# Kernel tuning notes

Hardware: AMD Instinct MI355X
Metric: run time of the kernel (lower is better)

Reference implementation:

```python
import jax, jax.numpy as jnp
import numpy as np

N_NODES = 50000
E_EDGES = 800000
NODE_DIM = 64
HID = 128


def _leaky(x):
    return jnp.where(x > 0, x, 0.2 * x)


def _gat_conv(x, W, a_src, a_dst, b, src, dst, heads, out_ch, concat):
    # x: [N, in]; W: [in, heads*out]; a_src/a_dst: [heads, out]
    N = x.shape[0]
    h = (x @ W).reshape(N, heads, out_ch)            # [N, H, C]
    s = (h * a_src[None]).sum(-1)                    # [N, H]
    d = (h * a_dst[None]).sum(-1)                    # [N, H]
    e = _leaky(s[src] + d[dst])                      # [E, H]
    m = jax.ops.segment_max(e, dst, num_segments=N)  # segment softmax (stable)
    ex = jnp.exp(e - m[dst])
    denom = jax.ops.segment_sum(ex, dst, num_segments=N)
    alpha = ex / denom[dst]                          # [E, H] (self-loops -> denom>0)
    out = jax.ops.segment_sum(h[src] * alpha[..., None], dst, num_segments=N)
    out = out.reshape(N, heads * out_ch) if concat else out.mean(axis=1)
    return out + b


def setup_inputs() -> dict:
    key = jax.random.key(0)
    ks = jax.random.split(key, 16)
    sc = 0.1
    inp = {
        "x": jax.random.normal(ks[0], (N_NODES, NODE_DIM), jnp.float32),
        "edge_index": jax.random.randint(ks[1], (2, E_EDGES), 0, N_NODES, jnp.int64),
        "fc_w": jax.random.normal(ks[2], (NODE_DIM, HID), jnp.float32) * sc,
        "fc_b": jnp.zeros((HID,), jnp.float32),
        "W1": jax.random.normal(ks[3], (HID, 2 * HID), jnp.float32) * sc,
        "asrc1": jax.random.normal(ks[4], (2, HID), jnp.float32) * sc,
        "adst1": jax.random.normal(ks[5], (2, HID), jnp.float32) * sc,
        "b1": jnp.zeros((2 * HID,), jnp.float32),
        "Wm": jax.random.normal(ks[6], (4, 2 * HID, 2 * HID), jnp.float32) * sc,
        "asrcm": jax.random.normal(ks[7], (4, 2, HID), jnp.float32) * sc,
        "adstm": jax.random.normal(ks[8], (4, 2, HID), jnp.float32) * sc,
        "bm": jnp.zeros((4, 2 * HID), jnp.float32),
        "W6": jax.random.normal(ks[9], (2 * HID, HID), jnp.float32) * sc,
        "asrc6": jax.random.normal(ks[10], (1, HID), jnp.float32) * sc,
        "adst6": jax.random.normal(ks[11], (1, HID), jnp.float32) * sc,
        "b6": jnp.zeros((HID,), jnp.float32),
    }
    return inp


def reference(x, edge_index, fc_w, fc_b, W1, asrc1, adst1, b1,
              Wm, asrcm, adstm, bm, W6, asrc6, adst6, b6):
    N = x.shape[0]
    loops = jnp.arange(N, dtype=edge_index.dtype)
    src = jnp.concatenate([edge_index[0], loops])  # add_self_loops=True (PyG default)
    dst = jnp.concatenate([edge_index[1], loops])

    out = jax.nn.relu(x @ fc_w + fc_b)
    out = _gat_conv(out, W1, asrc1, adst1, b1, src, dst, 2, HID, True)
    for i in range(4):
        out = _gat_conv(out, Wm[i], asrcm[i], adstm[i], bm[i], src, dst, 2, HID, True)
    out = _gat_conv(out, W6, asrc6, adst6, b6, src, dst, 1, HID, True)
    return out
```

## Files before the change

kernel.cpp:

```cpp
#include <hip/hip_runtime.h>
#include <cstdint>
#include <cstddef>

#define NN 50000
#define EE 800000
#define ET 850000

typedef unsigned short ushort_t;
typedef unsigned int uint_t;
using frag_ab = __attribute__((ext_vector_type(8))) short;
using f32x4   = __attribute__((ext_vector_type(4))) float;

__device__ inline ushort_t f2b(float x) {
  union { float f; unsigned int u; } c; c.f = x;
  unsigned int u = c.u;
  u += 0x7fffu + ((u >> 16) & 1u);
  return (ushort_t)(u >> 16);
}
__device__ inline float b2f(uint_t u) {
  union { unsigned int u; float f; } c; c.u = u << 16;
  return c.f;
}

__global__ __launch_bounds__(256) void k_count(const int* __restrict__ edge,
                                               int* __restrict__ counts) {
  int e = blockIdx.x * 256 + threadIdx.x;
  if (e >= ET) return;
  int dd = (e < EE) ? edge[EE + e] : (e - EE);
  atomicAdd(&counts[dd], 1);
}

__global__ __launch_bounds__(1024) void k_scan1(const int* __restrict__ counts,
                                                int* __restrict__ scn,
                                                int* __restrict__ bsum) {
  __shared__ int tmp[1024];
  int tid = threadIdx.x;
  int idx = blockIdx.x * 1024 + tid;
  int v = (idx < NN) ? counts[idx] : 0;
  tmp[tid] = v;
  __syncthreads();
  for (int o = 1; o < 1024; o <<= 1) {
    int u = (tid >= o) ? tmp[tid - o] : 0;
    __syncthreads();
    tmp[tid] += u;
    __syncthreads();
  }
  if (idx < NN) scn[idx] = tmp[tid] - v;
  if (tid == 1023) bsum[blockIdx.x] = tmp[1023];
}

__global__ __launch_bounds__(64) void k_scan2(const int* __restrict__ bsum,
                                              int* __restrict__ boff) {
  int l = threadIdx.x;
  const int NB = (NN + 1023) / 1024;
  int v = (l < NB) ? bsum[l] : 0;
  int own = v;
  for (int o = 1; o < 64; o <<= 1) {
    int u = __shfl_up(v, o);
    if (l >= o) v += u;
  }
  if (l < NB) boff[l] = v - own;
}

__global__ __launch_bounds__(1024) void k_scan3(const int* __restrict__ scn,
                                                const int* __restrict__ boff,
                                                int* __restrict__ row_ptr,
                                                int* __restrict__ cursor) {
  int idx = blockIdx.x * 1024 + threadIdx.x;
  if (idx < NN) {
    int v = scn[idx] + boff[blockIdx.x];
    row_ptr[idx] = v;
    cursor[idx] = v;
  }
  if (idx == 0) row_ptr[NN] = ET;
}

__global__ __launch_bounds__(256) void k_fill(const int* __restrict__ edge,
                                              int* __restrict__ cursor,
                                              int* __restrict__ col_src) {
  int e = blockIdx.x * 256 + threadIdx.x;
  if (e >= ET) return;
  int ss, dd;
  if (e < EE) { ss = edge[e]; dd = edge[EE + e]; }
  else        { ss = dd = e - EE; }
  int pos = atomicAdd(&cursor[dd], 1);
  col_src[pos] = ss;
}

__global__ __launch_bounds__(256) void k_prep_w(const float* __restrict__ fc_w,
                                                const float* __restrict__ W1,
                                                const float* __restrict__ Wm,
                                                const float* __restrict__ W6,
                                                ushort_t* __restrict__ fcWt,
                                                ushort_t* __restrict__ W1t,
                                                ushort_t* __restrict__ Wmt,
                                                ushort_t* __restrict__ W6t) {
  int i = blockIdx.x * 256 + threadIdx.x;
  if (i < 128 * 64) { int n = i >> 6, k = i & 63; fcWt[i] = f2b(fc_w[k * 128 + n]); return; }
  i -= 128 * 64;
  if (i < 256 * 128) { int n = i >> 7, k = i & 127; W1t[i] = f2b(W1[k * 256 + n]); return; }
  i -= 256 * 128;
  if (i < 4 * 256 * 256) {
    int l = i >> 16, r2 = i & 65535, n = r2 >> 8, k = r2 & 255;
    Wmt[i] = f2b(Wm[(size_t)l * 65536 + k * 256 + n]); return;
  }
  i -= 4 * 256 * 256;
  if (i < 128 * 256) { int n = i >> 8, k = i & 255; W6t[i] = f2b(W6[k * 128 + n]); return; }
}

template<int ABF16, int RELU, int SD>
__global__ __launch_bounds__(256) void k_mfma_gemm(const void* __restrict__ A,
                                                   const ushort_t* __restrict__ Bt,
                                                   ushort_t* __restrict__ C,
                                                   int M, int K, int Nc,
                                                   const float* __restrict__ bias,
                                                   const float* __restrict__ a_src,
                                                   const float* __restrict__ a_dst,
                                                   float* __restrict__ sbuf,
                                                   float* __restrict__ dbuf,
                                                   int H) {
  __shared__ ushort_t As[128 * 40];
  __shared__ ushort_t Bs[128 * 40];
  __shared__ float sdred[128][2][2];
  int row0 = blockIdx.x * 128;
  int col0 = blockIdx.y * 128;
  int t = threadIdx.x;
  int lane = t & 63, w = t >> 6;
  int wr = w >> 1, wc = w & 1;
  int r = lane & 15, kg = lane >> 4;

  f32x4 acc[4][4];
#pragma unroll
  for (int m = 0; m < 4; ++m)
#pragma unroll
    for (int n = 0; n < 4; ++n) acc[m][n] = (f32x4){0.f, 0.f, 0.f, 0.f};

  for (int k0 = 0; k0 < K; k0 += 32) {
    __syncthreads();
    if (ABF16) {
#pragma unroll
      for (int rep = 0; rep < 2; ++rep) {
        int c = t + rep * 256;
        int row = c >> 2, kc = c & 3;
        int grow = row0 + row;
        if (grow < M) {
          uint4 v = *(const uint4*)&((const ushort_t*)A)[(size_t)grow * K + k0 + kc * 8];
          *(uint4*)&As[row * 40 + kc * 8] = v;
        }
      }
    } else {
#pragma unroll
      for (int rep = 0; rep < 4; ++rep) {
        int c = t + rep * 256;
        int row = c >> 3, kc = c & 7;
        int grow = row0 + row;
        if (grow < M) {
          float4 v = *(const float4*)&((const float*)A)[(size_t)grow * K + k0 + kc * 4];
          ushort4 u;
          u.x = f2b(v.x); u.y = f2b(v.y); u.z = f2b(v.z); u.w = f2b(v.w);
          *(ushort4*)&As[row * 40 + kc * 4] = u;
        }
      }
    }
#pragma unroll
    for (int rep = 0; rep < 2; ++rep) {
      int c = t + rep * 256;
      int row = c >> 2, kc = c & 3;
      uint4 v = *(const uint4*)&Bt[(size_t)(col0 + row) * K + k0 + kc * 8];
      *(uint4*)&Bs[row * 40 + kc * 8] = v;
    }
    __syncthreads();

    frag_ab a[4], b[4];
#pragma unroll
    for (int m = 0; m < 4; ++m)
      a[m] = *(const frag_ab*)&As[(wr * 64 + m * 16 + r) * 40 + kg * 8];
#pragma unroll
    for (int n = 0; n < 4; ++n)
      b[n] = *(const frag_ab*)&Bs[(wc * 64 + n * 16 + r) * 40 + kg * 8];
#pragma unroll
    for (int m = 0; m < 4; ++m)
#pragma unroll
      for (int n = 0; n < 4; ++n)
        acc[m][n] = __builtin_amdgcn_mfma_f32_16x16x32_bf16(a[m], b[n], acc[m][n], 0, 0, 0);
  }

  int head = blockIdx.y;
  float as_[4], ad_[4];
  if (SD) {
#pragma unroll
    for (int n = 0; n < 4; ++n) {
      int cloc = wc * 64 + n * 16 + r;
      as_[n] = a_src[head * 128 + cloc];
      ad_[n] = a_dst[head * 128 + cloc];
    }
  }

#pragma unroll
  for (int m = 0; m < 4; ++m) {
    int gr0 = row0 + wr * 64 + m * 16 + kg * 4;
#pragma unroll
    for (int q = 0; q < 4; ++q) {
      int grow = gr0 + q;
      float ps = 0.f, pd = 0.f;
      if (grow < M) {
#pragma unroll
        for (int n = 0; n < 4; ++n) {
          int gcol = col0 + wc * 64 + n * 16 + r;
          float val = acc[m][n][q];
          if (SD) { ps += val * as_[n]; pd += val * ad_[n]; }
          if (bias) val += bias[gcol];
          if (RELU) val = fmaxf(val, 0.f);
          C[(size_t)grow * Nc + gcol] = f2b(val);
        }
      }
      if (SD) {
#pragma unroll
        for (int o = 1; o < 16; o <<= 1) {
          ps += __shfl_xor(ps, o);
          pd += __shfl_xor(pd, o);
        }
        int row_loc = wr * 64 + m * 16 + kg * 4 + q;
        if (r == 0) { sdred[row_loc][wc][0] = ps; sdred[row_loc][wc][1] = pd; }
      }
    }
  }
  if (SD) {
    __syncthreads();
    int row = t >> 1, which = t & 1;
    int grow = row0 + row;
    if (grow < M) {
      float v = sdred[row][0][which] + sdred[row][1][which];
      float* dst = which ? dbuf : sbuf;
      dst[(size_t)grow * H + head] = v;
    }
  }
}

template<int H, int OUTBF>
__global__ __launch_bounds__(256) void k_agg(const ushort_t* __restrict__ h2,
                                             const float* __restrict__ s,
                                             const float* __restrict__ dv,
                                             const int* __restrict__ row_ptr,
                                             const int* __restrict__ col_src,
                                             const float* __restrict__ bias,
                                             void* __restrict__ out) {
  int wid = threadIdx.x >> 6, l = threadIdx.x & 63;
  int n = blockIdx.x * 4 + wid;
  if (n >= NN) return;
  int beg = row_ptr[n], end = row_ptr[n + 1];
  float dn0, dn1 = 0.f;
  if (H == 2) { float2 tdn = ((const float2*)dv)[n]; dn0 = tdn.x; dn1 = tdn.y; }
  else dn0 = dv[n];

  float m0 = -1e30f, d0 = 0.f, m1 = -1e30f, d1 = 0.f;
  for (int e = beg + l; e < end; e += 64) {
    int src = col_src[e];
    if (H == 2) {
      float2 sv = ((const float2*)s)[src];
      float x0 = sv.x + dn0; x0 = x0 > 0.f ? x0 : 0.2f * x0;
      if (x0 > m0) { d0 = d0 * __expf(m0 - x0) + 1.f; m0 = x0; } else d0 += __expf(x0 - m0);
      float x1 = sv.y + dn1; x1 = x1 > 0.f ? x1 : 0.2f * x1;
      if (x1 > m1) { d1 = d1 * __expf(m1 - x1) + 1.f; m1 = x1; } else d1 += __expf(x1 - m1);
    } else {
      float x0 = s[src] + dn0; x0 = x0 > 0.f ? x0 : 0.2f * x0;
      if (x0 > m0) { d0 = d0 * __expf(m0 - x0) + 1.f; m0 = x0; } else d0 += __expf(x0 - m0);
    }
  }
#pragma unroll
  for (int o = 1; o < 64; o <<= 1) {
    float mo = __shfl_xor(m0, o), dno = __shfl_xor(d0, o);
    float M2 = fmaxf(m0, mo);
    d0 = d0 * __expf(m0 - M2) + dno * __expf(mo - M2);
    m0 = M2;
    if (H == 2) {
      mo = __shfl_xor(m1, o); dno = __shfl_xor(d1, o);
      M2 = fmaxf(m1, mo);
      d1 = d1 * __expf(m1 - M2) + dno * __expf(mo - M2);
      m1 = M2;
    }
  }

  if (H == 2) {
    const uint2* hrow = (const uint2*)h2;
    int hh = l >> 5;
    float a0 = 0.f, a1 = 0.f, a2 = 0.f, a3 = 0.f;
    for (int c = beg; c < end; c += 32) {
      int cnt = min(32, end - c);
      float alpv = 0.f; int srcv = 0;
      if (l < 2 * cnt) {
        int e = c + (l >> 1), hi = l & 1;
        srcv = col_src[e];
        float x = s[srcv * 2 + hi] + (hi ? dn1 : dn0);
        x = x > 0.f ? x : 0.2f * x;
        alpv = __expf(x - (hi ? m1 : m0));
      }
      int e = 0;
      for (; e + 4 <= cnt; e += 4) {
        float p0 = __shfl(alpv, 2 * e + hh);     int s0 = __shfl(srcv, 2 * e);
        float p1 = __shfl(alpv, 2 * e + 2 + hh); int s1 = __shfl(srcv, 2 * e + 2);
        float p2 = __shfl(alpv, 2 * e + 4 + hh); int s2 = __shfl(srcv, 2 * e + 4);
        float p3 = __shfl(alpv, 2 * e + 6 + hh); int s3 = __shfl(srcv, 2 * e + 6);
        uint2 v0 = hrow[(size_t)s0 * 64 + l];
        uint2 v1 = hrow[(size_t)s1 * 64 + l];
        uint2 v2 = hrow[(size_t)s2 * 64 + l];
        uint2 v3 = hrow[(size_t)s3 * 64 + l];
        a0 += p0 * b2f(v0.x & 0xffffu); a1 += p0 * b2f(v0.x >> 16);
        a2 += p0 * b2f(v0.y & 0xffffu); a3 += p0 * b2f(v0.y >> 16);
        a0 += p1 * b2f(v1.x & 0xffffu); a1 += p1 * b2f(v1.x >> 16);
        a2 += p1 * b2f(v1.y & 0xffffu); a3 += p1 * b2f(v1.y >> 16);
        a0 += p2 * b2f(v2.x & 0xffffu); a1 += p2 * b2f(v2.x >> 16);
        a2 += p2 * b2f(v2.y & 0xffffu); a3 += p2 * b2f(v2.y >> 16);
        a0 += p3 * b2f(v3.x & 0xffffu); a1 += p3 * b2f(v3.x >> 16);
        a2 += p3 * b2f(v3.y & 0xffffu); a3 += p3 * b2f(v3.y >> 16);
      }
      for (; e < cnt; ++e) {
        float p = __shfl(alpv, 2 * e + hh); int sc = __shfl(srcv, 2 * e);
        uint2 v = hrow[(size_t)sc * 64 + l];
        a0 += p * b2f(v.x & 0xffffu); a1 += p * b2f(v.x >> 16);
        a2 += p * b2f(v.y & 0xffffu); a3 += p * b2f(v.y >> 16);
      }
    }
    float dh = hh ? d1 : d0;
    float4 bb = ((const float4*)bias)[l];
    float o0 = a0 / dh + bb.x, o1 = a1 / dh + bb.y;
    float o2 = a2 / dh + bb.z, o3 = a3 / dh + bb.w;
    if (OUTBF) {
      uint2 ov;
      ov.x = (uint_t)f2b(o0) | ((uint_t)f2b(o1) << 16);
      ov.y = (uint_t)f2b(o2) | ((uint_t)f2b(o3) << 16);
      ((uint2*)out)[(size_t)n * 64 + l] = ov;
    } else {
      ((float4*)out)[(size_t)n * 64 + l] = make_float4(o0, o1, o2, o3);
    }
  } else {
    const uint_t* hrow = (const uint_t*)h2;
    float a0 = 0.f, a1 = 0.f;
    for (int c = beg; c < end; c += 64) {
      int cnt = min(64, end - c);
      float alpv = 0.f; int srcv = 0;
      if (l < cnt) {
        srcv = col_src[c + l];
        float x = s[srcv] + dn0;
        x = x > 0.f ? x : 0.2f * x;
        alpv = __expf(x - m0);
      }
      int e = 0;
      for (; e + 4 <= cnt; e += 4) {
        float p0 = __shfl(alpv, e);     int s0 = __shfl(srcv, e);
        float p1 = __shfl(alpv, e + 1); int s1 = __shfl(srcv, e + 1);
        float p2 = __shfl(alpv, e + 2); int s2 = __shfl(srcv, e + 2);
        float p3 = __shfl(alpv, e + 3); int s3 = __shfl(srcv, e + 3);
        uint_t v0 = hrow[(size_t)s0 * 64 + l];
        uint_t v1 = hrow[(size_t)s1 * 64 + l];
        uint_t v2 = hrow[(size_t)s2 * 64 + l];
        uint_t v3 = hrow[(size_t)s3 * 64 + l];
        a0 += p0 * b2f(v0 & 0xffffu); a1 += p0 * b2f(v0 >> 16);
        a0 += p1 * b2f(v1 & 0xffffu); a1 += p1 * b2f(v1 >> 16);
        a0 += p2 * b2f(v2 & 0xffffu); a1 += p2 * b2f(v2 >> 16);
        a0 += p3 * b2f(v3 & 0xffffu); a1 += p3 * b2f(v3 >> 16);
      }
      for (; e < cnt; ++e) {
        float p = __shfl(alpv, e); int sc = __shfl(srcv, e);
        uint_t v = hrow[(size_t)sc * 64 + l];
        a0 += p * b2f(v & 0xffffu); a1 += p * b2f(v >> 16);
      }
    }
    float2 bb = ((const float2*)bias)[l];
    float o0 = a0 / d0 + bb.x, o1 = a1 / d0 + bb.y;
    if (OUTBF) {
      ((uint_t*)out)[(size_t)n * 64 + l] = (uint_t)f2b(o0) | ((uint_t)f2b(o1) << 16);
    } else {
      ((float2*)out)[(size_t)n * 64 + l] = make_float2(o0, o1);
    }
  }
}

extern "C" void kernel_launch(void* const* d_in, const int* in_sizes, int n_in,
                              void* d_out, int out_size, void* d_ws, size_t ws_size,
                              hipStream_t stream) {
  const float* x     = (const float*)d_in[0];
  const int*   edge  = (const int*)d_in[1];
  const float* fc_w  = (const float*)d_in[2];
  const float* fc_b  = (const float*)d_in[3];
  const float* W1    = (const float*)d_in[4];
  const float* asrc1 = (const float*)d_in[5];
  const float* adst1 = (const float*)d_in[6];
  const float* b1    = (const float*)d_in[7];
  const float* Wm    = (const float*)d_in[8];
  const float* asrcm = (const float*)d_in[9];
  const float* adstm = (const float*)d_in[10];
  const float* bm    = (const float*)d_in[11];
  const float* W6    = (const float*)d_in[12];
  const float* asrc6 = (const float*)d_in[13];
  const float* adst6 = (const float*)d_in[14];
  const float* b6    = (const float*)d_in[15];

  char* w = (char*)d_ws;
  size_t off = 0;
  auto carve = [&](size_t bytes) -> char* {
    char* p = w + off;
    off = (off + bytes + 255) & ~(size_t)255;
    return p;
  };
  ushort_t* feat0 = (ushort_t*)carve((size_t)NN * 256 * 2);
  ushort_t* feat1 = (ushort_t*)carve((size_t)NN * 256 * 2);
  ushort_t* hbuf  = (ushort_t*)carve((size_t)NN * 256 * 2);
  float* sbuf   = (float*)carve((size_t)NN * 2 * 4);
  float* dbuf   = (float*)carve((size_t)NN * 2 * 4);
  ushort_t* fcWt = (ushort_t*)carve((size_t)128 * 64 * 2);
  ushort_t* W1t  = (ushort_t*)carve((size_t)256 * 128 * 2);
  ushort_t* Wmt  = (ushort_t*)carve((size_t)4 * 256 * 256 * 2);
  ushort_t* W6t  = (ushort_t*)carve((size_t)128 * 256 * 2);
  int* counts   = (int*)carve((size_t)NN * 4);
  int* row_ptr  = (int*)carve((size_t)(NN + 1) * 4);
  int* cursor   = (int*)carve((size_t)NN * 4);
  int* col_src  = (int*)carve((size_t)ET * 4);
  int* scn      = (int*)carve((size_t)NN * 4);
  int* bsum     = (int*)carve((size_t)64 * 4);
  int* boff     = (int*)carve((size_t)64 * 4);
  (void)ws_size;

  k_prep_w<<<(335872 + 255) / 256, 256, 0, stream>>>(fc_w, W1, Wm, W6, fcWt, W1t, Wmt, W6t);

  hipMemsetAsync(counts, 0, (size_t)NN * 4, stream);
  int eb = (ET + 255) / 256;
  const int NB = (NN + 1023) / 1024;
  k_count<<<eb, 256, 0, stream>>>(edge, counts);
  k_scan1<<<NB, 1024, 0, stream>>>(counts, scn, bsum);
  k_scan2<<<1, 64, 0, stream>>>(bsum, boff);
  k_scan3<<<NB, 1024, 0, stream>>>(scn, boff, row_ptr, cursor);
  k_fill<<<eb, 256, 0, stream>>>(edge, cursor, col_src);

  dim3 g1((NN + 127) / 128, 1), g2((NN + 127) / 128, 2);
  int ab = (NN + 3) / 4;

  auto gat = [&](const ushort_t* in, int K, const ushort_t* Wt, const float* a_s,
                 const float* a_d, const float* bias, void* outp, int H, int outbf) {
    k_mfma_gemm<1, 0, 1><<<(H == 2 ? g2 : g1), 256, 0, stream>>>(
        in, Wt, hbuf, NN, K, H * 128, nullptr, a_s, a_d, sbuf, dbuf, H);
    if (H == 2) {
      if (outbf)
        k_agg<2, 1><<<ab, 256, 0, stream>>>(hbuf, sbuf, dbuf, row_ptr, col_src, bias, outp);
      else
        k_agg<2, 0><<<ab, 256, 0, stream>>>(hbuf, sbuf, dbuf, row_ptr, col_src, bias, outp);
    } else {
      if (outbf)
        k_agg<1, 1><<<ab, 256, 0, stream>>>(hbuf, sbuf, dbuf, row_ptr, col_src, bias, outp);
      else
        k_agg<1, 0><<<ab, 256, 0, stream>>>(hbuf, sbuf, dbuf, row_ptr, col_src, bias, outp);
    }
  };

  k_mfma_gemm<0, 1, 0><<<g1, 256, 0, stream>>>(x, fcWt, feat0, NN, 64, 128, fc_b,
                                               nullptr, nullptr, nullptr, nullptr, 1);

  gat(feat0, 128, W1t, asrc1, adst1, b1, feat1, 2, 1);

  const ushort_t* cur = feat1;
  ushort_t* nxt = feat0;
  for (int i = 0; i < 4; ++i) {
    gat(cur, 256, Wmt + (size_t)i * 256 * 256, asrcm + (size_t)i * 2 * 128,
        adstm + (size_t)i * 2 * 128, bm + (size_t)i * 256, nxt, 2, 1);
    const ushort_t* tmp = cur;
    cur = nxt;
    nxt = (ushort_t*)tmp;
  }

  gat(cur, 256, W6t, asrc6, adst6, b6, d_out, 1, 0);
}
```

Baseline: 659.1 us.

## Use direct-to-LDS loads with swizzle in GEMM and 16-byte gathers in aggregation

The bf16 GEMM now uses K-tiles of 64 and loads A/B tiles straight into LDS with global_load_lds. Those tiles use an XOR-swizzled layout in place of padding, to cut register staging and LDS bank conflicts. The aggregation kernels now gather 16-byte rows per lane, with two or four edges processed in parallel across half- or quarter-wavefronts, then reduce across lanes with shuffles. This aims to lower the number of memory transactions in the edge gather, at the cost of an extra cross-lane reduction and idle lanes at the final store.

```diff
diff --git a/kernel.cpp b/kernel.cpp
--- a/kernel.cpp
+++ b/kernel.cpp
@@ -20,6 +20,12 @@
 __device__ inline float b2f(uint_t u) {
   union { unsigned int u; float f; } c; c.u = u << 16;
   return c.f;
+}
+
+__device__ inline void gload16(const ushort_t* g, ushort_t* l) {
+  __builtin_amdgcn_global_load_lds(
+      (const __attribute__((address_space(1))) unsigned int*)g,
+      (__attribute__((address_space(3))) unsigned int*)l, 16, 0, 0);
 }
 
 __global__ __launch_bounds__(256) void k_count(const int* __restrict__ edge,
@@ -108,19 +114,92 @@
   if (i < 128 * 256) { int n = i >> 8, k = i & 255; W6t[i] = f2b(W6[k * 128 + n]); return; }
 }
 
-template<int ABF16, int RELU, int SD>
-__global__ __launch_bounds__(256) void k_mfma_gemm(const void* __restrict__ A,
-                                                   const ushort_t* __restrict__ Bt,
-                                                   ushort_t* __restrict__ C,
-                                                   int M, int K, int Nc,
-                                                   const float* __restrict__ bias,
-                                                   const float* __restrict__ a_src,
-                                                   const float* __restrict__ a_dst,
-                                                   float* __restrict__ sbuf,
-                                                   float* __restrict__ dbuf,
-                                                   int H) {
+__global__ __launch_bounds__(256) void k_gemm_f32(const float* __restrict__ A,
+                                                  const ushort_t* __restrict__ Bt,
+                                                  ushort_t* __restrict__ C,
+                                                  int M, int K, int Nc,
+                                                  const float* __restrict__ bias) {
   __shared__ ushort_t As[128 * 40];
   __shared__ ushort_t Bs[128 * 40];
+  int row0 = blockIdx.x * 128;
+  int col0 = blockIdx.y * 128;
+  int t = threadIdx.x;
+  int lane = t & 63, w = t >> 6;
+  int wr = w >> 1, wc = w & 1;
+  int r = lane & 15, kg = lane >> 4;
+
+  f32x4 acc[4][4];
+#pragma unroll
+  for (int m = 0; m < 4; ++m)
+#pragma unroll
+    for (int n = 0; n < 4; ++n) acc[m][n] = (f32x4){0.f, 0.f, 0.f, 0.f};
+
+  for (int k0 = 0; k0 < K; k0 += 32) {
+    __syncthreads();
+#pragma unroll
+    for (int rep = 0; rep < 4; ++rep) {
+      int c = t + rep * 256;
+      int row = c >> 3, kc = c & 7;
+      int grow = row0 + row;
+      if (grow < M) {
+        float4 v = *(const float4*)&A[(size_t)grow * K + k0 + kc * 4];
+        ushort4 u;
+        u.x = f2b(v.x); u.y = f2b(v.y); u.z = f2b(v.z); u.w = f2b(v.w);
+        *(ushort4*)&As[row * 40 + kc * 4] = u;
+      }
+    }
+#pragma unroll
+    for (int rep = 0; rep < 2; ++rep) {
+      int c = t + rep * 256;
+      int row = c >> 2, kc = c & 3;
+      uint4 v = *(const uint4*)&Bt[(size_t)(col0 + row) * K + k0 + kc * 8];
+      *(uint4*)&Bs[row * 40 + kc * 8] = v;
+    }
+    __syncthreads();
+
+    frag_ab a[4], b[4];
+#pragma unroll
+    for (int m = 0; m < 4; ++m)
+      a[m] = *(const frag_ab*)&As[(wr * 64 + m * 16 + r) * 40 + kg * 8];
+#pragma unroll
+    for (int n = 0; n < 4; ++n)
+      b[n] = *(const frag_ab*)&Bs[(wc * 64 + n * 16 + r) * 40 + kg * 8];
+#pragma unroll
+    for (int m = 0; m < 4; ++m)
+#pragma unroll
+      for (int n = 0; n < 4; ++n)
+        acc[m][n] = __builtin_amdgcn_mfma_f32_16x16x32_bf16(a[m], b[n], acc[m][n], 0, 0, 0);
+  }
+
+#pragma unroll
+  for (int m = 0; m < 4; ++m) {
+    int gr0 = row0 + wr * 64 + m * 16 + kg * 4;
+#pragma unroll
+    for (int q = 0; q < 4; ++q) {
+      int grow = gr0 + q;
+      if (grow >= M) continue;
+#pragma unroll
+      for (int n = 0; n < 4; ++n) {
+        int gcol = col0 + wc * 64 + n * 16 + r;
+        float val = acc[m][n][q] + bias[gcol];
+        val = fmaxf(val, 0.f);
+        C[(size_t)grow * Nc + gcol] = f2b(val);
+      }
+    }
+  }
+}
+
+__global__ __launch_bounds__(256) void k_gemm64(const ushort_t* __restrict__ A,
+                                                const ushort_t* __restrict__ Bt,
+                                                ushort_t* __restrict__ C,
+                                                int M, int K, int Nc,
+                                                const float* __restrict__ a_src,
+                                                const float* __restrict__ a_dst,
+                                                float* __restrict__ sbuf,
+                                                float* __restrict__ dbuf,
+                                                int H) {
+  __shared__ ushort_t As[128 * 64];
+  __shared__ ushort_t Bs[128 * 64];
   __shared__ float sdred[128][2][2];
   int row0 = blockIdx.x * 128;
   int col0 = blockIdx.y * 128;
@@ -135,65 +214,51 @@
 #pragma unroll
     for (int n = 0; n < 4; ++n) acc[m][n] = (f32x4){0.f, 0.f, 0.f, 0.f};
 
-  for (int k0 = 0; k0 < K; k0 += 32) {
+  for (int k0 = 0; k0 < K; k0 += 64) {
     __syncthreads();
-    if (ABF16) {
-#pragma unroll
-      for (int rep = 0; rep < 2; ++rep) {
-        int c = t + rep * 256;
-        int row = c >> 2, kc = c & 3;
-        int grow = row0 + row;
-        if (grow < M) {
-          uint4 v = *(const uint4*)&((const ushort_t*)A)[(size_t)grow * K + k0 + kc * 8];
-          *(uint4*)&As[row * 40 + kc * 8] = v;
-        }
+#pragma unroll
+    for (int i = 0; i < 4; ++i) {
+      int c = w * 4 + i;
+      int b = c * 1024 + lane * 16;
+      int row = b >> 7;
+      int ks = ((b >> 4) & 7) ^ (row & 7);
+      const ushort_t* ga = A + (size_t)(row0 + row) * K + k0 + ks * 8;
+      if (row0 + row < M) gload16(ga, &As[c * 512]);
+      const ushort_t* gb = Bt + (size_t)(col0 + row) * K + k0 + ks * 8;
+      gload16(gb, &Bs[c * 512]);
+    }
+    __syncthreads();
+
+#pragma unroll
+    for (int kk = 0; kk < 2; ++kk) {
+      frag_ab af[4], bf[4];
+#pragma unroll
+      for (int m = 0; m < 4; ++m) {
+        int row = wr * 64 + m * 16 + r;
+        int byte = row * 128 + ((kk * 64 + kg * 16) ^ ((row & 7) << 4));
+        af[m] = *(const frag_ab*)((const char*)As + byte);
       }
-    } else {
-#pragma unroll
-      for (int rep = 0; rep < 4; ++rep) {
-        int c = t + rep * 256;
-        int row = c >> 3, kc = c & 7;
-        int grow = row0 + row;
-        if (grow < M) {
-          float4 v = *(const float4*)&((const float*)A)[(size_t)grow * K + k0 + kc * 4];
-          ushort4 u;
-          u.x = f2b(v.x); u.y = f2b(v.y); u.z = f2b(v.z); u.w = f2b(v.w);
-          *(ushort4*)&As[row * 40 + kc * 4] = u;
-        }
+#pragma unroll
+      for (int n = 0; n < 4; ++n) {
+        int row = wc * 64 + n * 16 + r;
+        int byte = row * 128 + ((kk * 64 + kg * 16) ^ ((row & 7) << 4));
+        bf[n] = *(const frag_ab*)((const char*)Bs + byte);
       }
-    }
-#pragma unroll
-    for (int rep = 0; rep < 2; ++rep) {
-      int c = t + rep * 256;
-      int row = c >> 2, kc = c & 3;
-      uint4 v = *(const uint4*)&Bt[(size_t)(col0 + row) * K + k0 + kc * 8];
-      *(uint4*)&Bs[row * 40 + kc * 8] = v;
-    }
-    __syncthreads();
-
-    frag_ab a[4], b[4];
-#pragma unroll
-    for (int m = 0; m < 4; ++m)
-      a[m] = *(const frag_ab*)&As[(wr * 64 + m * 16 + r) * 40 + kg * 8];
-#pragma unroll
-    for (int n = 0; n < 4; ++n)
-      b[n] = *(const frag_ab*)&Bs[(wc * 64 + n * 16 + r) * 40 + kg * 8];
-#pragma unroll
-    for (int m = 0; m < 4; ++m)
-#pragma unroll
-      for (int n = 0; n < 4; ++n)
-        acc[m][n] = __builtin_amdgcn_mfma_f32_16x16x32_bf16(a[m], b[n], acc[m][n], 0, 0, 0);
+#pragma unroll
+      for (int m = 0; m < 4; ++m)
+#pragma unroll
+        for (int n = 0; n < 4; ++n)
+          acc[m][n] = __builtin_amdgcn_mfma_f32_16x16x32_bf16(af[m], bf[n], acc[m][n], 0, 0, 0);
+    }
   }
 
   int head = blockIdx.y;
   float as_[4], ad_[4];
-  if (SD) {
-#pragma unroll
-    for (int n = 0; n < 4; ++n) {
-      int cloc = wc * 64 + n * 16 + r;
-      as_[n] = a_src[head * 128 + cloc];
-      ad_[n] = a_dst[head * 128 + cloc];
-    }
+#pragma unroll
+  for (int n = 0; n < 4; ++n) {
+    int cloc = wc * 64 + n * 16 + r;
+    as_[n] = a_src[head * 128 + cloc];
+    ad_[n] = a_dst[head * 128 + cloc];
   }
 
 #pragma unroll
@@ -208,64 +273,51 @@
         for (int n = 0; n < 4; ++n) {
           int gcol = col0 + wc * 64 + n * 16 + r;
           float val = acc[m][n][q];
-          if (SD) { ps += val * as_[n]; pd += val * ad_[n]; }
-          if (bias) val += bias[gcol];
-          if (RELU) val = fmaxf(val, 0.f);
+          ps += val * as_[n]; pd += val * ad_[n];
           C[(size_t)grow * Nc + gcol] = f2b(val);
         }
       }
-      if (SD) {
-#pragma unroll
-        for (int o = 1; o < 16; o <<= 1) {
-          ps += __shfl_xor(ps, o);
-          pd += __shfl_xor(pd, o);
-        }
-        int row_loc = wr * 64 + m * 16 + kg * 4 + q;
-        if (r == 0) { sdred[row_loc][wc][0] = ps; sdred[row_loc][wc][1] = pd; }
+#pragma unroll
+      for (int o = 1; o < 16; o <<= 1) {
+        ps += __shfl_xor(ps, o);
+        pd += __shfl_xor(pd, o);
       }
-    }
-  }
-  if (SD) {
-    __syncthreads();
-    int row = t >> 1, which = t & 1;
-    int grow = row0 + row;
-    if (grow < M) {
-      float v = sdred[row][0][which] + sdred[row][1][which];
-      float* dst = which ? dbuf : sbuf;
-      dst[(size_t)grow * H + head] = v;
-    }
-  }
-}
-
-template<int H, int OUTBF>
-__global__ __launch_bounds__(256) void k_agg(const ushort_t* __restrict__ h2,
-                                             const float* __restrict__ s,
-                                             const float* __restrict__ dv,
-                                             const int* __restrict__ row_ptr,
-                                             const int* __restrict__ col_src,
-                                             const float* __restrict__ bias,
-                                             void* __restrict__ out) {
+      int row_loc = wr * 64 + m * 16 + kg * 4 + q;
+      if (r == 0) { sdred[row_loc][wc][0] = ps; sdred[row_loc][wc][1] = pd; }
+    }
+  }
+  __syncthreads();
+  int row = t >> 1, which = t & 1;
+  int grow = row0 + row;
+  if (grow < M) {
+    float v = sdred[row][0][which] + sdred[row][1][which];
+    float* dst = which ? dbuf : sbuf;
+    dst[(size_t)grow * H + head] = v;
+  }
+}
+
+__global__ __launch_bounds__(256) void k_agg2(const ushort_t* __restrict__ h2,
+                                              const float* __restrict__ s,
+                                              const float* __restrict__ dv,
+                                              const int* __restrict__ row_ptr,
+                                              const int* __restrict__ col_src,
+                                              const float* __restrict__ bias,
+                                              uint4* __restrict__ out) {
   int wid = threadIdx.x >> 6, l = threadIdx.x & 63;
   int n = blockIdx.x * 4 + wid;
   if (n >= NN) return;
   int beg = row_ptr[n], end = row_ptr[n + 1];
-  float dn0, dn1 = 0.f;
-  if (H == 2) { float2 tdn = ((const float2*)dv)[n]; dn0 = tdn.x; dn1 = tdn.y; }
-  else dn0 = dv[n];
+  float2 tdn = ((const float2*)dv)[n];
+  float dn0 = tdn.x, dn1 = tdn.y;
 
   float m0 = -1e30f, d0 = 0.f, m1 = -1e30f, d1 = 0.f;
   for (int e = beg + l; e < end; e += 64) {
     int src = col_src[e];
-    if (H == 2) {
-      float2 sv = ((const float2*)s)[src];
-      float x0 = sv.x + dn0; x0 = x0 > 0.f ? x0 : 0.2f * x0;
-      if (x0 > m0) { d0 = d0 * __expf(m0 - x0) + 1.f; m0 = x0; } else d0 += __expf(x0 - m0);
-      float x1 = sv.y + dn1; x1 = x1 > 0.f ? x1 : 0.2f * x1;
-      if (x1 > m1) { d1 = d1 * __expf(m1 - x1) + 1.f; m1 = x1; } else d1 += __expf(x1 - m1);
-    } else {
-      float x0 = s[src] + dn0; x0 = x0 > 0.f ? x0 : 0.2f * x0;
-      if (x0 > m0) { d0 = d0 * __expf(m0 - x0) + 1.f; m0 = x0; } else d0 += __expf(x0 - m0);
-    }
+    float2 sv = ((const float2*)s)[src];
+    float x0 = sv.x + dn0; x0 = x0 > 0.f ? x0 : 0.2f * x0;
+    if (x0 > m0) { d0 = d0 * __expf(m0 - x0) + 1.f; m0 = x0; } else d0 += __expf(x0 - m0);
+    float x1 = sv.y + dn1; x1 = x1 > 0.f ? x1 : 0.2f * x1;
+    if (x1 > m1) { d1 = d1 * __expf(m1 - x1) + 1.f; m1 = x1; } else d1 += __expf(x1 - m1);
   }
 #pragma unroll
   for (int o = 1; o < 64; o <<= 1) {
@@ -273,106 +325,147 @@
     float M2 = fmaxf(m0, mo);
     d0 = d0 * __expf(m0 - M2) + dno * __expf(mo - M2);
     m0 = M2;
-    if (H == 2) {
-      mo = __shfl_xor(m1, o); dno = __shfl_xor(d1, o);
-      M2 = fmaxf(m1, mo);
-      d1 = d1 * __expf(m1 - M2) + dno * __expf(mo - M2);
-      m1 = M2;
-    }
-  }
-
-  if (H == 2) {
-    const uint2* hrow = (const uint2*)h2;
-    int hh = l >> 5;
-    float a0 = 0.f, a1 = 0.f, a2 = 0.f, a3 = 0.f;
-    for (int c = beg; c < end; c += 32) {
-      int cnt = min(32, end - c);
-      float alpv = 0.f; int srcv = 0;
-      if (l < 2 * cnt) {
-        int e = c + (l >> 1), hi = l & 1;
-        srcv = col_src[e];
-        float x = s[srcv * 2 + hi] + (hi ? dn1 : dn0);
-        x = x > 0.f ? x : 0.2f * x;
-        alpv = __expf(x - (hi ? m1 : m0));
-      }
-      int e = 0;
-      for (; e + 4 <= cnt; e += 4) {
-        float p0 = __shfl(alpv, 2 * e + hh);     int s0 = __shfl(srcv, 2 * e);
-        float p1 = __shfl(alpv, 2 * e + 2 + hh); int s1 = __shfl(srcv, 2 * e + 2);
-        float p2 = __shfl(alpv, 2 * e + 4 + hh); int s2 = __shfl(srcv, 2 * e + 4);
-        float p3 = __shfl(alpv, 2 * e + 6 + hh); int s3 = __shfl(srcv, 2 * e + 6);
-        uint2 v0 = hrow[(size_t)s0 * 64 + l];
-        uint2 v1 = hrow[(size_t)s1 * 64 + l];
-        uint2 v2 = hrow[(size_t)s2 * 64 + l];
-        uint2 v3 = hrow[(size_t)s3 * 64 + l];
-        a0 += p0 * b2f(v0.x & 0xffffu); a1 += p0 * b2f(v0.x >> 16);
-        a2 += p0 * b2f(v0.y & 0xffffu); a3 += p0 * b2f(v0.y >> 16);
-        a0 += p1 * b2f(v1.x & 0xffffu); a1 += p1 * b2f(v1.x >> 16);
-        a2 += p1 * b2f(v1.y & 0xffffu); a3 += p1 * b2f(v1.y >> 16);
-        a0 += p2 * b2f(v2.x & 0xffffu); a1 += p2 * b2f(v2.x >> 16);
-        a2 += p2 * b2f(v2.y & 0xffffu); a3 += p2 * b2f(v2.y >> 16);
-        a0 += p3 * b2f(v3.x & 0xffffu); a1 += p3 * b2f(v3.x >> 16);
-        a2 += p3 * b2f(v3.y & 0xffffu); a3 += p3 * b2f(v3.y >> 16);
-      }
-      for (; e < cnt; ++e) {
-        float p = __shfl(alpv, 2 * e + hh); int sc = __shfl(srcv, 2 * e);
-        uint2 v = hrow[(size_t)sc * 64 + l];
-        a0 += p * b2f(v.x & 0xffffu); a1 += p * b2f(v.x >> 16);
-        a2 += p * b2f(v.y & 0xffffu); a3 += p * b2f(v.y >> 16);
-      }
-    }
-    float dh = hh ? d1 : d0;
-    float4 bb = ((const float4*)bias)[l];
-    float o0 = a0 / dh + bb.x, o1 = a1 / dh + bb.y;
-    float o2 = a2 / dh + bb.z, o3 = a3 / dh + bb.w;
-    if (OUTBF) {
-      uint2 ov;
-      ov.x = (uint_t)f2b(o0) | ((uint_t)f2b(o1) << 16);
-      ov.y = (uint_t)f2b(o2) | ((uint_t)f2b(o3) << 16);
-      ((uint2*)out)[(size_t)n * 64 + l] = ov;
-    } else {
-      ((float4*)out)[(size_t)n * 64 + l] = make_float4(o0, o1, o2, o3);
-    }
-  } else {
-    const uint_t* hrow = (const uint_t*)h2;
-    float a0 = 0.f, a1 = 0.f;
-    for (int c = beg; c < end; c += 64) {
-      int cnt = min(64, end - c);
-      float alpv = 0.f; int srcv = 0;
-      if (l < cnt) {
-        srcv = col_src[c + l];
-        float x = s[srcv] + dn0;
-        x = x > 0.f ? x : 0.2f * x;
-        alpv = __expf(x - m0);
-      }
-      int e = 0;
-      for (; e + 4 <= cnt; e += 4) {
-        float p0 = __shfl(alpv, e);     int s0 = __shfl(srcv, e);
-        float p1 = __shfl(alpv, e + 1); int s1 = __shfl(srcv, e + 1);
-        float p2 = __shfl(alpv, e + 2); int s2 = __shfl(srcv, e + 2);
-        float p3 = __shfl(alpv, e + 3); int s3 = __shfl(srcv, e + 3);
-        uint_t v0 = hrow[(size_t)s0 * 64 + l];
-        uint_t v1 = hrow[(size_t)s1 * 64 + l];
-        uint_t v2 = hrow[(size_t)s2 * 64 + l];
-        uint_t v3 = hrow[(size_t)s3 * 64 + l];
-        a0 += p0 * b2f(v0 & 0xffffu); a1 += p0 * b2f(v0 >> 16);
-        a0 += p1 * b2f(v1 & 0xffffu); a1 += p1 * b2f(v1 >> 16);
-        a0 += p2 * b2f(v2 & 0xffffu); a1 += p2 * b2f(v2 >> 16);
-        a0 += p3 * b2f(v3 & 0xffffu); a1 += p3 * b2f(v3 >> 16);
-      }
-      for (; e < cnt; ++e) {
-        float p = __shfl(alpv, e); int sc = __shfl(srcv, e);
-        uint_t v = hrow[(size_t)sc * 64 + l];
-        a0 += p * b2f(v & 0xffffu); a1 += p * b2f(v >> 16);
-      }
-    }
-    float2 bb = ((const float2*)bias)[l];
-    float o0 = a0 / d0 + bb.x, o1 = a1 / d0 + bb.y;
-    if (OUTBF) {
-      ((uint_t*)out)[(size_t)n * 64 + l] = (uint_t)f2b(o0) | ((uint_t)f2b(o1) << 16);
-    } else {
-      ((float2*)out)[(size_t)n * 64 + l] = make_float2(o0, o1);
-    }
+    mo = __shfl_xor(m1, o); dno = __shfl_xor(d1, o);
+    M2 = fmaxf(m1, mo);
+    d1 = d1 * __expf(m1 - M2) + dno * __expf(mo - M2);
+    m1 = M2;
+  }
+
+  int hw = l >> 5, lh = l & 31;
+  int hd = lh >> 4;
+  const uint4* hrow = (const uint4*)h2;
+  float a0 = 0.f, a1 = 0.f, a2 = 0.f, a3 = 0.f;
+  float a4 = 0.f, a5 = 0.f, a6 = 0.f, a7 = 0.f;
+
+  for (int c = beg; c < end; c += 32) {
+    int cnt = min(32, end - c);
+    float alpv = 0.f; int srcv = 0;
+    if (l < 2 * cnt) {
+      int e = c + (l >> 1), hi = l & 1;
+      srcv = col_src[e];
+      float x = s[srcv * 2 + hi] + (hi ? dn1 : dn0);
+      x = x > 0.f ? x : 0.2f * x;
+      alpv = __expf(x - (hi ? m1 : m0));
+    }
+    int e = 0;
+    for (; e + 4 <= cnt + 1; e += 4) {
+      int ep0 = e + hw, ep1 = e + 2 + hw;
+      int s0 = __shfl(srcv, 2 * ep0);
+      int s1 = __shfl(srcv, 2 * ep1);
+      float p0 = __shfl(alpv, 2 * ep0 + hd);
+      float p1 = __shfl(alpv, 2 * ep1 + hd);
+      if (ep0 >= cnt) p0 = 0.f;
+      if (ep1 >= cnt) p1 = 0.f;
+      uint4 v0 = hrow[(size_t)s0 * 32 + lh];
+      uint4 v1 = hrow[(size_t)s1 * 32 + lh];
+      a0 = fmaf(p0, b2f(v0.x & 0xffffu), a0); a1 = fmaf(p0, b2f(v0.x >> 16), a1);
+      a2 = fmaf(p0, b2f(v0.y & 0xffffu), a2); a3 = fmaf(p0, b2f(v0.y >> 16), a3);
+      a4 = fmaf(p0, b2f(v0.z & 0xffffu), a4); a5 = fmaf(p0, b2f(v0.z >> 16), a5);
+      a6 = fmaf(p0, b2f(v0.w & 0xffffu), a6); a7 = fmaf(p0, b2f(v0.w >> 16), a7);
+      a0 = fmaf(p1, b2f(v1.x & 0xffffu), a0); a1 = fmaf(p1, b2f(v1.x >> 16), a1);
+      a2 = fmaf(p1, b2f(v1.y & 0xffffu), a2); a3 = fmaf(p1, b2f(v1.y >> 16), a3);
+      a4 = fmaf(p1, b2f(v1.z & 0xffffu), a4); a5 = fmaf(p1, b2f(v1.z >> 16), a5);
+      a6 = fmaf(p1, b2f(v1.w & 0xffffu), a6); a7 = fmaf(p1, b2f(v1.w >> 16), a7);
+    }
+    for (; e < cnt; e += 2) {
+      int ep = e + hw;
+      int s0 = __shfl(srcv, 2 * ep);
+      float p = __shfl(alpv, 2 * ep + hd);
+      if (ep >= cnt) p = 0.f;
+      uint4 v = hrow[(size_t)s0 * 32 + lh];
+      a0 = fmaf(p, b2f(v.x & 0xffffu), a0); a1 = fmaf(p, b2f(v.x >> 16), a1);
+      a2 = fmaf(p, b2f(v.y & 0xffffu), a2); a3 = fmaf(p, b2f(v.y >> 16), a3);
+      a4 = fmaf(p, b2f(v.z & 0xffffu), a4); a5 = fmaf(p, b2f(v.z >> 16), a5);
+      a6 = fmaf(p, b2f(v.w & 0xffffu), a6); a7 = fmaf(p, b2f(v.w >> 16), a7);
+    }
+  }
+  a0 += __shfl_xor(a0, 32); a1 += __shfl_xor(a1, 32);
+  a2 += __shfl_xor(a2, 32); a3 += __shfl_xor(a3, 32);
+  a4 += __shfl_xor(a4, 32); a5 += __shfl_xor(a5, 32);
+  a6 += __shfl_xor(a6, 32); a7 += __shfl_xor(a7, 32);
+
+  if (hw == 0) {
+    float dh = hd ? d1 : d0;
+    float inv = 1.f / dh;
+    float4 b0 = ((const float4*)bias)[2 * lh];
+    float4 b1 = ((const float4*)bias)[2 * lh + 1];
+    uint4 ov;
+    ov.x = (uint_t)f2b(a0 * inv + b0.x) | ((uint_t)f2b(a1 * inv + b0.y) << 16);
+    ov.y = (uint_t)f2b(a2 * inv + b0.z) | ((uint_t)f2b(a3 * inv + b0.w) << 16);
+    ov.z = (uint_t)f2b(a4 * inv + b1.x) | ((uint_t)f2b(a5 * inv + b1.y) << 16);
+    ov.w = (uint_t)f2b(a6 * inv + b1.z) | ((uint_t)f2b(a7 * inv + b1.w) << 16);
+    out[(size_t)n * 32 + lh] = ov;
+  }
+}
+
+__global__ __launch_bounds__(256) void k_agg1(const ushort_t* __restrict__ h2,
+                                              const float* __restrict__ s,
+                                              const float* __restrict__ dv,
+                                              const int* __restrict__ row_ptr,
+                                              const int* __restrict__ col_src,
+                                              const float* __restrict__ bias,
+                                              float* __restrict__ out) {
+  int wid = threadIdx.x >> 6, l = threadIdx.x & 63;
+  int n = blockIdx.x * 4 + wid;
+  if (n >= NN) return;
+  int beg = row_ptr[n], end = row_ptr[n + 1];
+  float dn0 = dv[n];
+
+  float m0 = -1e30f, d0 = 0.f;
+  for (int e = beg + l; e < end; e += 64) {
+    float x0 = s[col_src[e]] + dn0;
+    x0 = x0 > 0.f ? x0 : 0.2f * x0;
+    if (x0 > m0) { d0 = d0 * __expf(m0 - x0) + 1.f; m0 = x0; } else d0 += __expf(x0 - m0);
+  }
+#pragma unroll
+  for (int o = 1; o < 64; o <<= 1) {
+    float mo = __shfl_xor(m0, o), dno = __shfl_xor(d0, o);
+    float M2 = fmaxf(m0, mo);
+    d0 = d0 * __expf(m0 - M2) + dno * __expf(mo - M2);
+    m0 = M2;
+  }
+
+  int hw = l >> 4, lh = l & 15;
+  const uint4* hrow = (const uint4*)h2;
+  float a0 = 0.f, a1 = 0.f, a2 = 0.f, a3 = 0.f;
+  float a4 = 0.f, a5 = 0.f, a6 = 0.f, a7 = 0.f;
+
+  for (int c = beg; c < end; c += 64) {
+    int cnt = min(64, end - c);
+    float alpv = 0.f; int srcv = 0;
+    if (l < cnt) {
+      srcv = col_src[c + l];
+      float x = s[srcv] + dn0;
+      x = x > 0.f ? x : 0.2f * x;
+      alpv = __expf(x - m0);
+    }
+    for (int e = 0; e < cnt; e += 4) {
+      int ep = e + hw;
+      int s0 = __shfl(srcv, ep);
+      float p = __shfl(alpv, ep);
+      if (ep >= cnt) p = 0.f;
+      uint4 v = hrow[(size_t)s0 * 16 + lh];
+      a0 = fmaf(p, b2f(v.x & 0xffffu), a0); a1 = fmaf(p, b2f(v.x >> 16), a1);
+      a2 = fmaf(p, b2f(v.y & 0xffffu), a2); a3 = fmaf(p, b2f(v.y >> 16), a3);
+      a4 = fmaf(p, b2f(v.z & 0xffffu), a4); a5 = fmaf(p, b2f(v.z >> 16), a5);
+      a6 = fmaf(p, b2f(v.w & 0xffffu), a6); a7 = fmaf(p, b2f(v.w >> 16), a7);
+    }
+  }
+#pragma unroll
+  for (int o = 16; o < 64; o <<= 1) {
+    a0 += __shfl_xor(a0, o); a1 += __shfl_xor(a1, o);
+    a2 += __shfl_xor(a2, o); a3 += __shfl_xor(a3, o);
+    a4 += __shfl_xor(a4, o); a5 += __shfl_xor(a5, o);
+    a6 += __shfl_xor(a6, o); a7 += __shfl_xor(a7, o);
+  }
+  if (hw == 0) {
+    float inv = 1.f / d0;
+    float4 b0 = ((const float4*)bias)[2 * lh];
+    float4 b1 = ((const float4*)bias)[2 * lh + 1];
+    float4 o0 = make_float4(a0 * inv + b0.x, a1 * inv + b0.y, a2 * inv + b0.z, a3 * inv + b0.w);
+    float4 o1 = make_float4(a4 * inv + b1.x, a5 * inv + b1.y, a6 * inv + b1.z, a7 * inv + b1.w);
+    ((float4*)out)[(size_t)n * 32 + 2 * lh] = o0;
+    ((float4*)out)[(size_t)n * 32 + 2 * lh + 1] = o1;
   }
 }
 
@@ -436,36 +529,28 @@
   int ab = (NN + 3) / 4;
 
   auto gat = [&](const ushort_t* in, int K, const ushort_t* Wt, const float* a_s,
-                 const float* a_d, const float* bias, void* outp, int H, int outbf) {
-    k_mfma_gemm<1, 0, 1><<<(H == 2 ? g2 : g1), 256, 0, stream>>>(
-        in, Wt, hbuf, NN, K, H * 128, nullptr, a_s, a_d, sbuf, dbuf, H);
-    if (H == 2) {
-      if (outbf)
-        k_agg<2, 1><<<ab, 256, 0, stream>>>(hbuf, sbuf, dbuf, row_ptr, col_src, bias, outp);
-      else
-        k_agg<2, 0><<<ab, 256, 0, stream>>>(hbuf, sbuf, dbuf, row_ptr, col_src, bias, outp);
-    } else {
-      if (outbf)
-        k_agg<1, 1><<<ab, 256, 0, stream>>>(hbuf, sbuf, dbuf, row_ptr, col_src, bias, outp);
-      else
-        k_agg<1, 0><<<ab, 256, 0, stream>>>(hbuf, sbuf, dbuf, row_ptr, col_src, bias, outp);
-    }
+                 const float* a_d, const float* bias, void* outp, int H) {
+    k_gemm64<<<(H == 2 ? g2 : g1), 256, 0, stream>>>(
+        in, Wt, hbuf, NN, K, H * 128, a_s, a_d, sbuf, dbuf, H);
+    if (H == 2)
+      k_agg2<<<ab, 256, 0, stream>>>(hbuf, sbuf, dbuf, row_ptr, col_src, bias, (uint4*)outp);
+    else
+      k_agg1<<<ab, 256, 0, stream>>>(hbuf, sbuf, dbuf, row_ptr, col_src, bias, (float*)outp);
   };
 
-  k_mfma_gemm<0, 1, 0><<<g1, 256, 0, stream>>>(x, fcWt, feat0, NN, 64, 128, fc_b,
-                                               nullptr, nullptr, nullptr, nullptr, 1);
-
-  gat(feat0, 128, W1t, asrc1, adst1, b1, feat1, 2, 1);
+  k_gemm_f32<<<g1, 256, 0, stream>>>(x, fcWt, feat0, NN, 64, 128, fc_b);
+
+  gat(feat0, 128, W1t, asrc1, adst1, b1, feat1, 2);
 
   const ushort_t* cur = feat1;
   ushort_t* nxt = feat0;
   for (int i = 0; i < 4; ++i) {
     gat(cur, 256, Wmt + (size_t)i * 256 * 256, asrcm + (size_t)i * 2 * 128,
-        adstm + (size_t)i * 2 * 128, bm + (size_t)i * 256, nxt, 2, 1);
+        adstm + (size_t)i * 2 * 128, bm + (size_t)i * 256, nxt, 2);
     const ushort_t* tmp = cur;
     cur = nxt;
     nxt = (ushort_t*)tmp;
   }
 
-  gat(cur, 256, W6t, asrc6, adst6, b6, d_out, 1, 0);
-}
+  gat(cur, 256, W6t, asrc6, adst6, b6, d_out, 1);
+}
```

Measured after the change: 599.3 us. -9.1%, faster.
